# Performance work log

Measured on AMD Instinct MI355X. Metric: run time of the kernel, lower is better.

The kernel has to match this reference:

```python
import jax, jax.numpy as jnp
import numpy as np

B, T, F, H = 8192, 96, 64, 256


def setup_inputs() -> dict:
    key = jax.random.key(0)
    ks = jax.random.split(key, 8)
    s = 0.05
    return {
        "decoder_feature": jax.random.normal(ks[0], (B, T, F), jnp.float32),
        "init_state": jax.random.normal(ks[1], (B, H), jnp.float32),
        "decoder_init_input": jax.random.normal(ks[2], (B, 1), jnp.float32),
        "kernel": jax.random.normal(ks[3], (1 + F, 3 * H), jnp.float32) * s,
        "recurrent_kernel": jax.random.normal(ks[4], (H, 3 * H), jnp.float32) * s,
        "input_bias": jnp.zeros((3 * H,), jnp.float32),
        "recurrent_bias": jnp.zeros((3 * H,), jnp.float32),
        "dense_w": jax.random.normal(ks[5], (H, 1), jnp.float32) * s,
        "dense_b": jnp.zeros((1,), jnp.float32),
        "predict_seq_length": T,
    }


def reference(decoder_feature, init_state, decoder_init_input, kernel,
              recurrent_kernel, input_bias, recurrent_bias, dense_w, dense_b,
              predict_seq_length):
    # teacher=None, use_attention=False path of Decoder2.forward.
    # Keras GRUCell (reset_after=True) recurrence, scanned over time.
    feats = jnp.swapaxes(decoder_feature[:, :predict_seq_length, :], 0, 1)  # [T,B,F]

    def step(carry, feat_t):
        prev_out, h = carry                                   # [B,1], [B,H]
        x = jnp.concatenate([prev_out, feat_t], axis=-1)      # [B,1+F]
        mx = x @ kernel + input_bias                          # [B,3H]
        mh = h @ recurrent_kernel + recurrent_bias            # [B,3H]
        xz, xr, xh = jnp.split(mx, 3, axis=-1)
        hz, hr, hh = jnp.split(mh, 3, axis=-1)
        z = jax.nn.sigmoid(xz + hz)
        r = jax.nn.sigmoid(xr + hr)
        cand = jnp.tanh(xh + r * hh)
        h_new = z * h + (1.0 - z) * cand
        out = h_new @ dense_w + dense_b                       # [B,1]
        return (out, h_new), out

    _, outs = jax.lax.scan(step, (decoder_init_input, init_state), feats)
    return jnp.swapaxes(outs, 0, 1)                           # [B,T,1]
```

## Files before the change

kernel.cpp:

```cpp
#include <hip/hip_runtime.h>


#define Bdim 8192
#define Tdim 96
#define Fdim 64
#define Hdim 256
#define BM   32
#define XS   104
#define HS   264

typedef __attribute__((ext_vector_type(8))) short s16x8;
typedef __attribute__((ext_vector_type(4))) float f32x4;

#define MFMA __builtin_amdgcn_mfma_f32_16x16x32_bf16

__device__ __forceinline__ unsigned short f2bf(float f) {
    union { float f; unsigned u; } v; v.f = f;
    unsigned r = v.u + 0x7FFFu + ((v.u >> 16) & 1u);
    return (unsigned short)(r >> 16);
}

__global__ void prep_swz(const float* __restrict__ Wk, const float* __restrict__ Wr,
                         unsigned short* __restrict__ sK, unsigned short* __restrict__ sR) {
    int idx = blockIdx.x * blockDim.x + threadIdx.x;
    if (idx < 24576) {
        int lane = idx & 63, rest = idx >> 6;
        int nt = rest % 6; rest /= 6;
        int kt = rest % 8; int w = rest / 8;
        int q = lane >> 4, cc = lane & 15;
        int n = (nt >> 1) * 256 + w * 32 + (nt & 1) * 16 + cc;
        unsigned short* d = sR + (size_t)idx * 8;
#pragma unroll
        for (int j = 0; j < 8; ++j) {
            int k = kt * 32 + q * 8 + j;
            d[j] = f2bf(Wr[(size_t)k * 768 + n]);
        }
    } else if (idx < 24576 + 9216) {
        int i2 = idx - 24576;
        int lane = i2 & 63, rest = i2 >> 6;
        int nt = rest % 6; rest /= 6;
        int kt = rest % 3; int w = rest / 3;
        int q = lane >> 4, cc = lane & 15;
        int n = (nt >> 1) * 256 + w * 32 + (nt & 1) * 16 + cc;
        unsigned short* d = sK + (size_t)i2 * 8;
#pragma unroll
        for (int j = 0; j < 8; ++j) {
            int k = kt * 32 + q * 8 + j;
            float v = (k < 64) ? Wk[(size_t)(k + 1) * 768 + n]
                               : (k == 64 ? Wk[n] : 0.0f);
            d[j] = f2bf(v);
        }
    }
}

__launch_bounds__(512, 2)
__global__ void gru_mfma(
    const float* __restrict__ feat,
    const float* __restrict__ init_state,
    const float* __restrict__ init_inp,
    const unsigned short* __restrict__ sK,
    const unsigned short* __restrict__ sR,
    const float* __restrict__ ib, const float* __restrict__ rb,
    const float* __restrict__ dw, const float* __restrict__ db,
    float* __restrict__ out)
{
    __shared__ __align__(16) unsigned short xs[BM * XS];
    __shared__ __align__(16) unsigned short hs[BM * HS];
    __shared__ float wpart[8][BM];

    const int tid  = threadIdx.x;
    const int lane = tid & 63;
    const int w    = tid >> 6;
    const int q    = lane >> 4;
    const int c    = lane & 15;
    const int b0   = blockIdx.x * BM;

    for (int i = tid; i < BM * XS; i += 512) xs[i] = 0;
    __syncthreads();

    float bz[2], brr[2], bxh[2], bhh[2], dwv[2];
#pragma unroll
    for (int n2 = 0; n2 < 2; ++n2) {
        int col = w * 32 + n2 * 16 + c;
        bz[n2]  = ib[col] + rb[col];
        brr[n2] = ib[256 + col] + rb[256 + col];
        bxh[n2] = ib[512 + col];
        bhh[n2] = rb[512 + col];
        dwv[n2] = dw[col];
    }
    const float dbv = db[0];

    float hreg[2][2][4];
#pragma unroll
    for (int mt = 0; mt < 2; ++mt)
#pragma unroll
        for (int n2 = 0; n2 < 2; ++n2)
#pragma unroll
            for (int i = 0; i < 4; ++i) {
                int row = mt * 16 + q * 4 + i;
                int col = w * 32 + n2 * 16 + c;
                float v = init_state[(size_t)(b0 + row) * Hdim + col];
                hreg[mt][n2][i] = v;
                hs[row * HS + col] = f2bf(v);
            }

    {
        int r = tid >> 4, fi = tid & 15;
        float4 f = *(const float4*)&feat[((size_t)(b0 + r) * Tdim + 0) * Fdim + fi * 4];
        ushort4 p; p.x = f2bf(f.x); p.y = f2bf(f.y); p.z = f2bf(f.z); p.w = f2bf(f.w);
        *(ushort4*)&xs[r * XS + fi * 4] = p;
    }
    if (tid < BM) xs[tid * XS + 64] = f2bf(init_inp[b0 + tid]);

    s16x8 wk[3][6];
    {
        const unsigned short* kp = sK + (size_t)w * 3 * 6 * 512 + lane * 8;
#pragma unroll
        for (int kt = 0; kt < 3; ++kt)
#pragma unroll
            for (int nt = 0; nt < 6; ++nt)
                wk[kt][nt] = *(const s16x8*)(kp + (kt * 6 + nt) * 512);
    }
    const unsigned short* wrp = sR + (size_t)w * 8 * 6 * 512 + lane * 8;

    __syncthreads();

    for (int t = 0; t < Tdim; ++t) {
        f32x4 az[2][2], arr[2][2], axh[2][2], ahh[2][2];
#pragma unroll
        for (int mt = 0; mt < 2; ++mt)
#pragma unroll
            for (int n2 = 0; n2 < 2; ++n2) {
                az[mt][n2] = (f32x4)0.0f; arr[mt][n2] = (f32x4)0.0f;
                axh[mt][n2] = (f32x4)0.0f; ahh[mt][n2] = (f32x4)0.0f;
            }

#pragma unroll
        for (int kt = 0; kt < 3; ++kt) {
            s16x8 a0 = *(const s16x8*)&xs[c * XS + kt * 32 + q * 8];
            s16x8 a1 = *(const s16x8*)&xs[(16 + c) * XS + kt * 32 + q * 8];
            az[0][0]  = MFMA(a0, wk[kt][0], az[0][0], 0, 0, 0);
            az[1][0]  = MFMA(a1, wk[kt][0], az[1][0], 0, 0, 0);
            az[0][1]  = MFMA(a0, wk[kt][1], az[0][1], 0, 0, 0);
            az[1][1]  = MFMA(a1, wk[kt][1], az[1][1], 0, 0, 0);
            arr[0][0] = MFMA(a0, wk[kt][2], arr[0][0], 0, 0, 0);
            arr[1][0] = MFMA(a1, wk[kt][2], arr[1][0], 0, 0, 0);
            arr[0][1] = MFMA(a0, wk[kt][3], arr[0][1], 0, 0, 0);
            arr[1][1] = MFMA(a1, wk[kt][3], arr[1][1], 0, 0, 0);
            axh[0][0] = MFMA(a0, wk[kt][4], axh[0][0], 0, 0, 0);
            axh[1][0] = MFMA(a1, wk[kt][4], axh[1][0], 0, 0, 0);
            axh[0][1] = MFMA(a0, wk[kt][5], axh[0][1], 0, 0, 0);
            axh[1][1] = MFMA(a1, wk[kt][5], axh[1][1], 0, 0, 0);
        }

#pragma unroll
        for (int kt = 0; kt < 8; ++kt) {
            s16x8 b[6];
#pragma unroll
            for (int nt = 0; nt < 6; ++nt)
                b[nt] = *(const s16x8*)(wrp + (size_t)(kt * 6 + nt) * 512);
            s16x8 a0 = *(const s16x8*)&hs[c * HS + kt * 32 + q * 8];
            s16x8 a1 = *(const s16x8*)&hs[(16 + c) * HS + kt * 32 + q * 8];
            az[0][0]  = MFMA(a0, b[0], az[0][0], 0, 0, 0);
            az[1][0]  = MFMA(a1, b[0], az[1][0], 0, 0, 0);
            az[0][1]  = MFMA(a0, b[1], az[0][1], 0, 0, 0);
            az[1][1]  = MFMA(a1, b[1], az[1][1], 0, 0, 0);
            arr[0][0] = MFMA(a0, b[2], arr[0][0], 0, 0, 0);
            arr[1][0] = MFMA(a1, b[2], arr[1][0], 0, 0, 0);
            arr[0][1] = MFMA(a0, b[3], arr[0][1], 0, 0, 0);
            arr[1][1] = MFMA(a1, b[3], arr[1][1], 0, 0, 0);
            ahh[0][0] = MFMA(a0, b[4], ahh[0][0], 0, 0, 0);
            ahh[1][0] = MFMA(a1, b[4], ahh[1][0], 0, 0, 0);
            ahh[0][1] = MFMA(a0, b[5], ahh[0][1], 0, 0, 0);
            ahh[1][1] = MFMA(a1, b[5], ahh[1][1], 0, 0, 0);
        }
        __syncthreads();

        float sdense[2][4];
#pragma unroll
        for (int mt = 0; mt < 2; ++mt)
#pragma unroll
            for (int i = 0; i < 4; ++i) sdense[mt][i] = 0.0f;

#pragma unroll
        for (int mt = 0; mt < 2; ++mt)
#pragma unroll
            for (int n2 = 0; n2 < 2; ++n2)
#pragma unroll
                for (int i = 0; i < 4; ++i) {
                    float zz = 1.0f / (1.0f + __expf(-(az[mt][n2][i] + bz[n2])));
                    float rr = 1.0f / (1.0f + __expf(-(arr[mt][n2][i] + brr[n2])));
                    float cd = tanhf(axh[mt][n2][i] + bxh[n2] +
                                     rr * (ahh[mt][n2][i] + bhh[n2]));
                    float hn = zz * hreg[mt][n2][i] + (1.0f - zz) * cd;
                    hreg[mt][n2][i] = hn;
                    int row = mt * 16 + q * 4 + i;
                    int col = w * 32 + n2 * 16 + c;
                    hs[row * HS + col] = f2bf(hn);
                    sdense[mt][i] += hn * dwv[n2];
                }

#pragma unroll
        for (int mt = 0; mt < 2; ++mt)
#pragma unroll
            for (int i = 0; i < 4; ++i) {
                float s = sdense[mt][i];
                s += __shfl_xor(s, 1, 64);
                s += __shfl_xor(s, 2, 64);
                s += __shfl_xor(s, 4, 64);
                s += __shfl_xor(s, 8, 64);
                if (c == 0) wpart[w][mt * 16 + q * 4 + i] = s;
            }

        if (t + 1 < Tdim) {
            int r = tid >> 4, fi = tid & 15;
            float4 f = *(const float4*)&feat[((size_t)(b0 + r) * Tdim + (t + 1)) * Fdim + fi * 4];
            ushort4 p; p.x = f2bf(f.x); p.y = f2bf(f.y); p.z = f2bf(f.z); p.w = f2bf(f.w);
            *(ushort4*)&xs[r * XS + fi * 4] = p;
        }
        __syncthreads();

        if (tid < BM) {
            float s = dbv;
#pragma unroll
            for (int ww = 0; ww < 8; ++ww) s += wpart[ww][tid];
            out[(size_t)(b0 + tid) * Tdim + t] = s;
            xs[tid * XS + 64] = f2bf(s);
        }
        __syncthreads();
    }
}

extern "C" void kernel_launch(void* const* d_in, const int* in_sizes, int n_in,
                              void* d_out, int out_size, void* d_ws, size_t ws_size,
                              hipStream_t stream) {
    const float* feat       = (const float*)d_in[0];
    const float* init_state = (const float*)d_in[1];
    const float* init_inp   = (const float*)d_in[2];
    const float* Wk         = (const float*)d_in[3];
    const float* Wr         = (const float*)d_in[4];
    const float* ib         = (const float*)d_in[5];
    const float* rb         = (const float*)d_in[6];
    const float* dw         = (const float*)d_in[7];
    const float* db         = (const float*)d_in[8];
    float* out              = (float*)d_out;

    unsigned short* sR = (unsigned short*)d_ws;
    unsigned short* sK = (unsigned short*)((char*)d_ws + 24576 * 16);

    prep_swz<<<(24576 + 9216 + 255) / 256, 256, 0, stream>>>(Wk, Wr, sK, sR);
    gru_mfma<<<Bdim / BM, 512, 0, stream>>>(
        feat, init_state, init_inp, sK, sR, ib, rb, dw, db, out);
}
```

Baseline: 1.848 ms.

## Split GRU hidden columns over 16 waves and fold feedback into a scalar term

Blocks grow to 1024 threads (16 waves), so each wave owns 16 hidden columns instead of 32, which halves per-wave MFMA and weight-register work per step. The previous-output feedback input is taken out of the bf16 MFMA and applied as an fp32 scalar multiply with the first kernel row, shrinking the input K dimension from 96 to 64. The dense reduction is computed redundantly by every wave at the start of the next step, removing one barrier per timestep. Outputs are staged in shared memory and written coalesced at the end. In exchange, occupancy and register limits change and more wave-level synchronisation is needed per block.

```diff
diff --git a/kernel.cpp b/kernel.cpp
--- a/kernel.cpp
+++ b/kernel.cpp
@@ -6,8 +6,9 @@
 #define Fdim 64
 #define Hdim 256
 #define BM   32
-#define XS   104
+#define XS   72
 #define HS   264
+#define OS   97
 
 typedef __attribute__((ext_vector_type(8))) short s16x8;
 typedef __attribute__((ext_vector_type(4))) float f32x4;
@@ -23,50 +24,46 @@
 __global__ void prep_swz(const float* __restrict__ Wk, const float* __restrict__ Wr,
                          unsigned short* __restrict__ sK, unsigned short* __restrict__ sR) {
     int idx = blockIdx.x * blockDim.x + threadIdx.x;
+    int lane = idx & 63;
+    int q = lane >> 4, cc = lane & 15;
     if (idx < 24576) {
-        int lane = idx & 63, rest = idx >> 6;
-        int nt = rest % 6; rest /= 6;
-        int kt = rest % 8; int w = rest / 8;
-        int q = lane >> 4, cc = lane & 15;
-        int n = (nt >> 1) * 256 + w * 32 + (nt & 1) * 16 + cc;
+        int f = idx >> 6;
+        int g = f % 3; int rest = f / 3;
+        int kt = rest & 7; int w = rest >> 3;
+        int n = g * 256 + w * 16 + cc;
         unsigned short* d = sR + (size_t)idx * 8;
 #pragma unroll
-        for (int j = 0; j < 8; ++j) {
-            int k = kt * 32 + q * 8 + j;
-            d[j] = f2bf(Wr[(size_t)k * 768 + n]);
-        }
-    } else if (idx < 24576 + 9216) {
+        for (int j = 0; j < 8; ++j)
+            d[j] = f2bf(Wr[(size_t)(kt * 32 + q * 8 + j) * 768 + n]);
+    } else if (idx < 24576 + 6144) {
         int i2 = idx - 24576;
-        int lane = i2 & 63, rest = i2 >> 6;
-        int nt = rest % 6; rest /= 6;
-        int kt = rest % 3; int w = rest / 3;
-        int q = lane >> 4, cc = lane & 15;
-        int n = (nt >> 1) * 256 + w * 32 + (nt & 1) * 16 + cc;
+        int f = i2 >> 6;
+        int g = f % 3; int rest = f / 3;
+        int kt = rest & 1; int w = rest >> 1;
+        int n = g * 256 + w * 16 + cc;
         unsigned short* d = sK + (size_t)i2 * 8;
 #pragma unroll
-        for (int j = 0; j < 8; ++j) {
-            int k = kt * 32 + q * 8 + j;
-            float v = (k < 64) ? Wk[(size_t)(k + 1) * 768 + n]
-                               : (k == 64 ? Wk[n] : 0.0f);
-            d[j] = f2bf(v);
-        }
-    }
-}
-
-__launch_bounds__(512, 2)
-__global__ void gru_mfma(
+        for (int j = 0; j < 8; ++j)
+            d[j] = f2bf(Wk[(size_t)(1 + kt * 32 + q * 8 + j) * 768 + n]);
+    }
+}
+
+__launch_bounds__(1024, 4)
+__global__ void gru_mfma2(
     const float* __restrict__ feat,
     const float* __restrict__ init_state,
     const float* __restrict__ init_inp,
     const unsigned short* __restrict__ sK,
     const unsigned short* __restrict__ sR,
+    const float* __restrict__ Wk,
     const float* __restrict__ ib, const float* __restrict__ rb,
     const float* __restrict__ dw, const float* __restrict__ db,
     float* __restrict__ out)
 {
     __shared__ __align__(16) unsigned short xs[BM * XS];
     __shared__ __align__(16) unsigned short hs[BM * HS];
-    __shared__ float wpart[8][BM];
+    __shared__ float wpart[16][BM];
+    __shared__ float outbuf[BM * OS];
 
     const int tid  = threadIdx.x;
     const int lane = tid & 63;
@@ -75,159 +72,144 @@
     const int c    = lane & 15;
     const int b0   = blockIdx.x * BM;
 
-    for (int i = tid; i < BM * XS; i += 512) xs[i] = 0;
-    __syncthreads();
-
-    float bz[2], brr[2], bxh[2], bhh[2], dwv[2];
-#pragma unroll
-    for (int n2 = 0; n2 < 2; ++n2) {
-        int col = w * 32 + n2 * 16 + c;
-        bz[n2]  = ib[col] + rb[col];
-        brr[n2] = ib[256 + col] + rb[256 + col];
-        bxh[n2] = ib[512 + col];
-        bhh[n2] = rb[512 + col];
-        dwv[n2] = dw[col];
-    }
-    const float dbv = db[0];
-
-    float hreg[2][2][4];
+    const int colh = w * 16 + c;
+    const float bz   = ib[colh]       + rb[colh];
+    const float brr  = ib[256 + colh] + rb[256 + colh];
+    const float bxh  = ib[512 + colh];
+    const float bhh  = rb[512 + colh];
+    const float wk0z = Wk[colh], wk0r = Wk[256 + colh], wk0h = Wk[512 + colh];
+    const float dwv  = dw[colh];
+    const float dbv  = db[0];
+
+    float hreg[2][4];
+    float prevreg[2][4];
 #pragma unroll
     for (int mt = 0; mt < 2; ++mt)
 #pragma unroll
-        for (int n2 = 0; n2 < 2; ++n2)
-#pragma unroll
-            for (int i = 0; i < 4; ++i) {
-                int row = mt * 16 + q * 4 + i;
-                int col = w * 32 + n2 * 16 + c;
-                float v = init_state[(size_t)(b0 + row) * Hdim + col];
-                hreg[mt][n2][i] = v;
-                hs[row * HS + col] = f2bf(v);
-            }
-
-    {
+        for (int i = 0; i < 4; ++i) {
+            int row = mt * 16 + q * 4 + i;
+            float v = init_state[(size_t)(b0 + row) * Hdim + colh];
+            hreg[mt][i] = v;
+            hs[row * HS + colh] = f2bf(v);
+            prevreg[mt][i] = init_inp[b0 + row];
+        }
+
+    if (tid < 512) {
         int r = tid >> 4, fi = tid & 15;
         float4 f = *(const float4*)&feat[((size_t)(b0 + r) * Tdim + 0) * Fdim + fi * 4];
         ushort4 p; p.x = f2bf(f.x); p.y = f2bf(f.y); p.z = f2bf(f.z); p.w = f2bf(f.w);
         *(ushort4*)&xs[r * XS + fi * 4] = p;
     }
-    if (tid < BM) xs[tid * XS + 64] = f2bf(init_inp[b0 + tid]);
-
-    s16x8 wk[3][6];
+
+    s16x8 wkr[2][3];
     {
-        const unsigned short* kp = sK + (size_t)w * 3 * 6 * 512 + lane * 8;
-#pragma unroll
-        for (int kt = 0; kt < 3; ++kt)
-#pragma unroll
-            for (int nt = 0; nt < 6; ++nt)
-                wk[kt][nt] = *(const s16x8*)(kp + (kt * 6 + nt) * 512);
-    }
-    const unsigned short* wrp = sR + (size_t)w * 8 * 6 * 512 + lane * 8;
+        const unsigned short* kp = sK + (size_t)(w * 6) * 512 + lane * 8;
+#pragma unroll
+        for (int kt = 0; kt < 2; ++kt)
+#pragma unroll
+            for (int g = 0; g < 3; ++g)
+                wkr[kt][g] = *(const s16x8*)(kp + (kt * 3 + g) * 512);
+    }
+    const unsigned short* wrp = sR + (size_t)(w * 24) * 512 + lane * 8;
 
     __syncthreads();
 
     for (int t = 0; t < Tdim; ++t) {
-        f32x4 az[2][2], arr[2][2], axh[2][2], ahh[2][2];
-#pragma unroll
-        for (int mt = 0; mt < 2; ++mt)
-#pragma unroll
-            for (int n2 = 0; n2 < 2; ++n2) {
-                az[mt][n2] = (f32x4)0.0f; arr[mt][n2] = (f32x4)0.0f;
-                axh[mt][n2] = (f32x4)0.0f; ahh[mt][n2] = (f32x4)0.0f;
-            }
-
-#pragma unroll
-        for (int kt = 0; kt < 3; ++kt) {
+        if (t > 0) {
+            int r = lane & 31;
+            float s = dbv;
+#pragma unroll
+            for (int ww = 0; ww < 16; ++ww) s += wpart[ww][r];
+            if (w == 0 && lane < 32) outbuf[r * OS + (t - 1)] = s;
+#pragma unroll
+            for (int mt = 0; mt < 2; ++mt)
+#pragma unroll
+                for (int i = 0; i < 4; ++i)
+                    prevreg[mt][i] = __shfl(s, mt * 16 + q * 4 + i, 64);
+        }
+
+        f32x4 az[2], arr[2], axh[2], ahh[2];
+#pragma unroll
+        for (int mt = 0; mt < 2; ++mt) {
+            az[mt] = (f32x4)0.0f; arr[mt] = (f32x4)0.0f;
+            axh[mt] = (f32x4)0.0f; ahh[mt] = (f32x4)0.0f;
+        }
+
+#pragma unroll
+        for (int kt = 0; kt < 2; ++kt) {
             s16x8 a0 = *(const s16x8*)&xs[c * XS + kt * 32 + q * 8];
             s16x8 a1 = *(const s16x8*)&xs[(16 + c) * XS + kt * 32 + q * 8];
-            az[0][0]  = MFMA(a0, wk[kt][0], az[0][0], 0, 0, 0);
-            az[1][0]  = MFMA(a1, wk[kt][0], az[1][0], 0, 0, 0);
-            az[0][1]  = MFMA(a0, wk[kt][1], az[0][1], 0, 0, 0);
-            az[1][1]  = MFMA(a1, wk[kt][1], az[1][1], 0, 0, 0);
-            arr[0][0] = MFMA(a0, wk[kt][2], arr[0][0], 0, 0, 0);
-            arr[1][0] = MFMA(a1, wk[kt][2], arr[1][0], 0, 0, 0);
-            arr[0][1] = MFMA(a0, wk[kt][3], arr[0][1], 0, 0, 0);
-            arr[1][1] = MFMA(a1, wk[kt][3], arr[1][1], 0, 0, 0);
-            axh[0][0] = MFMA(a0, wk[kt][4], axh[0][0], 0, 0, 0);
-            axh[1][0] = MFMA(a1, wk[kt][4], axh[1][0], 0, 0, 0);
-            axh[0][1] = MFMA(a0, wk[kt][5], axh[0][1], 0, 0, 0);
-            axh[1][1] = MFMA(a1, wk[kt][5], axh[1][1], 0, 0, 0);
+            az[0]  = MFMA(a0, wkr[kt][0], az[0], 0, 0, 0);
+            az[1]  = MFMA(a1, wkr[kt][0], az[1], 0, 0, 0);
+            arr[0] = MFMA(a0, wkr[kt][1], arr[0], 0, 0, 0);
+            arr[1] = MFMA(a1, wkr[kt][1], arr[1], 0, 0, 0);
+            axh[0] = MFMA(a0, wkr[kt][2], axh[0], 0, 0, 0);
+            axh[1] = MFMA(a1, wkr[kt][2], axh[1], 0, 0, 0);
         }
 
 #pragma unroll
         for (int kt = 0; kt < 8; ++kt) {
-            s16x8 b[6];
-#pragma unroll
-            for (int nt = 0; nt < 6; ++nt)
-                b[nt] = *(const s16x8*)(wrp + (size_t)(kt * 6 + nt) * 512);
+            s16x8 bzf = *(const s16x8*)(wrp + (size_t)(kt * 3 + 0) * 512);
+            s16x8 brf = *(const s16x8*)(wrp + (size_t)(kt * 3 + 1) * 512);
+            s16x8 bhf = *(const s16x8*)(wrp + (size_t)(kt * 3 + 2) * 512);
             s16x8 a0 = *(const s16x8*)&hs[c * HS + kt * 32 + q * 8];
             s16x8 a1 = *(const s16x8*)&hs[(16 + c) * HS + kt * 32 + q * 8];
-            az[0][0]  = MFMA(a0, b[0], az[0][0], 0, 0, 0);
-            az[1][0]  = MFMA(a1, b[0], az[1][0], 0, 0, 0);
-            az[0][1]  = MFMA(a0, b[1], az[0][1], 0, 0, 0);
-            az[1][1]  = MFMA(a1, b[1], az[1][1], 0, 0, 0);
-            arr[0][0] = MFMA(a0, b[2], arr[0][0], 0, 0, 0);
-            arr[1][0] = MFMA(a1, b[2], arr[1][0], 0, 0, 0);
-            arr[0][1] = MFMA(a0, b[3], arr[0][1], 0, 0, 0);
-            arr[1][1] = MFMA(a1, b[3], arr[1][1], 0, 0, 0);
-            ahh[0][0] = MFMA(a0, b[4], ahh[0][0], 0, 0, 0);
-            ahh[1][0] = MFMA(a1, b[4], ahh[1][0], 0, 0, 0);
-            ahh[0][1] = MFMA(a0, b[5], ahh[0][1], 0, 0, 0);
-            ahh[1][1] = MFMA(a1, b[5], ahh[1][1], 0, 0, 0);
+            az[0]  = MFMA(a0, bzf, az[0], 0, 0, 0);
+            az[1]  = MFMA(a1, bzf, az[1], 0, 0, 0);
+            arr[0] = MFMA(a0, brf, arr[0], 0, 0, 0);
+            arr[1] = MFMA(a1, brf, arr[1], 0, 0, 0);
+            ahh[0] = MFMA(a0, bhf, ahh[0], 0, 0, 0);
+            ahh[1] = MFMA(a1, bhf, ahh[1], 0, 0, 0);
         }
         __syncthreads();
 
-        float sdense[2][4];
-#pragma unroll
-        for (int mt = 0; mt < 2; ++mt)
-#pragma unroll
-            for (int i = 0; i < 4; ++i) sdense[mt][i] = 0.0f;
-
-#pragma unroll
-        for (int mt = 0; mt < 2; ++mt)
-#pragma unroll
-            for (int n2 = 0; n2 < 2; ++n2)
-#pragma unroll
-                for (int i = 0; i < 4; ++i) {
-                    float zz = 1.0f / (1.0f + __expf(-(az[mt][n2][i] + bz[n2])));
-                    float rr = 1.0f / (1.0f + __expf(-(arr[mt][n2][i] + brr[n2])));
-                    float cd = tanhf(axh[mt][n2][i] + bxh[n2] +
-                                     rr * (ahh[mt][n2][i] + bhh[n2]));
-                    float hn = zz * hreg[mt][n2][i] + (1.0f - zz) * cd;
-                    hreg[mt][n2][i] = hn;
-                    int row = mt * 16 + q * 4 + i;
-                    int col = w * 32 + n2 * 16 + c;
-                    hs[row * HS + col] = f2bf(hn);
-                    sdense[mt][i] += hn * dwv[n2];
-                }
-
-#pragma unroll
-        for (int mt = 0; mt < 2; ++mt)
+#pragma unroll
+        for (int mt = 0; mt < 2; ++mt) {
+            float sd[4];
 #pragma unroll
             for (int i = 0; i < 4; ++i) {
-                float s = sdense[mt][i];
+                float pv = prevreg[mt][i];
+                float zz = 1.0f / (1.0f + __expf(-(az[mt][i] + bz + pv * wk0z)));
+                float rr = 1.0f / (1.0f + __expf(-(arr[mt][i] + brr + pv * wk0r)));
+                float cd = tanhf(axh[mt][i] + bxh + pv * wk0h +
+                                 rr * (ahh[mt][i] + bhh));
+                float hn = zz * hreg[mt][i] + (1.0f - zz) * cd;
+                hreg[mt][i] = hn;
+                hs[(mt * 16 + q * 4 + i) * HS + colh] = f2bf(hn);
+                sd[i] = hn * dwv;
+            }
+#pragma unroll
+            for (int i = 0; i < 4; ++i) {
+                float s = sd[i];
                 s += __shfl_xor(s, 1, 64);
                 s += __shfl_xor(s, 2, 64);
                 s += __shfl_xor(s, 4, 64);
                 s += __shfl_xor(s, 8, 64);
                 if (c == 0) wpart[w][mt * 16 + q * 4 + i] = s;
             }
-
-        if (t + 1 < Tdim) {
+        }
+
+        if (t + 1 < Tdim && tid < 512) {
             int r = tid >> 4, fi = tid & 15;
             float4 f = *(const float4*)&feat[((size_t)(b0 + r) * Tdim + (t + 1)) * Fdim + fi * 4];
             ushort4 p; p.x = f2bf(f.x); p.y = f2bf(f.y); p.z = f2bf(f.z); p.w = f2bf(f.w);
             *(ushort4*)&xs[r * XS + fi * 4] = p;
         }
         __syncthreads();
-
-        if (tid < BM) {
-            float s = dbv;
-#pragma unroll
-            for (int ww = 0; ww < 8; ++ww) s += wpart[ww][tid];
-            out[(size_t)(b0 + tid) * Tdim + t] = s;
-            xs[tid * XS + 64] = f2bf(s);
-        }
-        __syncthreads();
+    }
+
+    {
+        int r = lane & 31;
+        float s = dbv;
+#pragma unroll
+        for (int ww = 0; ww < 16; ++ww) s += wpart[ww][r];
+        if (w == 0 && lane < 32) outbuf[r * OS + (Tdim - 1)] = s;
+    }
+    __syncthreads();
+
+    for (int i = tid; i < BM * Tdim; i += 1024) {
+        int r = i / Tdim, tt = i - r * Tdim;
+        out[(size_t)b0 * Tdim + i] = outbuf[r * OS + tt];
     }
 }
 
@@ -248,7 +230,7 @@
     unsigned short* sR = (unsigned short*)d_ws;
     unsigned short* sK = (unsigned short*)((char*)d_ws + 24576 * 16);
 
-    prep_swz<<<(24576 + 9216 + 255) / 256, 256, 0, stream>>>(Wk, Wr, sK, sR);
-    gru_mfma<<<Bdim / BM, 512, 0, stream>>>(
-        feat, init_state, init_inp, sK, sR, ib, rb, dw, db, out);
-}
+    prep_swz<<<120, 256, 0, stream>>>(Wk, Wr, sK, sR);
+    gru_mfma2<<<Bdim / BM, 1024, 0, stream>>>(
+        feat, init_state, init_inp, sK, sR, Wk, ib, rb, dw, db, out);
+}
```

After: 1.935 ms. +4.7%, slower.
